# Optimization experiments

Measured on AMD Instinct MI355X. Metric: run time of the kernel, lower is better.

Reference implementation:

```python
import jax, jax.numpy as jnp
import numpy as np

GRID_SIZE = 16
NUM_VOXELS = GRID_SIZE ** 3


def setup_inputs() -> dict:
    key = jax.random.key(0)
    k1, k2, k3 = jax.random.split(key, 3)
    B, D, N = 4, 128, 100000
    features = jax.random.normal(k1, (B, D, N), dtype=jnp.float32)
    xyz_normalized = jax.random.uniform(k2, (B, N, 3), dtype=jnp.float32)
    mask = jax.random.randint(k3, (B, N), 0, 2, dtype=jnp.int32)
    return {"features": features, "xyz_normalized": xyz_normalized, "mask": mask}


def _flat_voxel_idx(xyz):
    # xyz: [B, N, 3] in [0,1); voxel index per point, flattened z*G*G + y*G + x
    G = GRID_SIZE
    vi = jnp.clip((xyz * G).astype(jnp.int32), 0, G - 1)  # [B, N, 3]
    return vi[..., 2] * (G * G) + vi[..., 1] * G + vi[..., 0]  # [B, N]


def reference(features, xyz_normalized, mask):
    # features: [B, D, N], xyz_normalized: [B, N, 3], mask: [B, N] int (0/1)
    idx = _flat_voxel_idx(xyz_normalized)  # [B, N]
    feats = features * mask[:, None, :].astype(features.dtype)  # [B, D, N]

    def per_batch(f_dn, idx_n, m_n):
        # scatter-add features: segment_sum over points -> [V, D] -> [D, V]
        sums = jax.ops.segment_sum(f_dn.T, idx_n, num_segments=NUM_VOXELS)  # [V, D]
        counts = jax.ops.segment_sum(m_n, idx_n, num_segments=NUM_VOXELS)  # [V]
        counts = jnp.maximum(counts, 1).astype(f_dn.dtype)
        return (sums / counts[:, None]).T  # [D, V]

    return jax.vmap(per_batch)(feats, idx, mask)  # [B, D, V]
```

## Files before the change

kernel.cpp:

```cpp
#include <hip/hip_runtime.h>

#define GSZ   16
#define NVOX  4096
#define BB    4
#define DD    128
#define PThr  256
#define PPT   16
#define PTILE (PThr * PPT)

typedef __fp16 half2v __attribute__((ext_vector_type(2)));

__device__ __forceinline__ void lds_pk_add_f16(unsigned byte_off, float va, float vb) {
    half2v h = __builtin_amdgcn_cvt_pkrtz(va, vb);
    unsigned hv;
    __builtin_memcpy(&hv, &h, 4);
    asm volatile("ds_pk_add_f16 %0, %1" : : "v"(byte_off), "v"(hv) : "memory");
}

__global__ __launch_bounds__(PThr) void k_prep(const float* __restrict__ xyz,
                                               const int* __restrict__ mask,
                                               unsigned short* __restrict__ idxm,
                                               unsigned short* __restrict__ histg,
                                               int N, int NT) {
    __shared__ unsigned int hist[NVOX];
    const int tile = blockIdx.x, b = blockIdx.y;
    for (int j = threadIdx.x; j < NVOX; j += PThr) hist[j] = 0u;
    __syncthreads();

    const float*    xb = xyz  + (size_t)b * N * 3;
    const int*      mb = mask + (size_t)b * N;
    unsigned short* ib = idxm + (size_t)b * N;

    const int p0 = tile * PTILE + (int)threadIdx.x * PPT;

    if (p0 + PPT <= N) {
        float a[3 * PPT];
        float4* av = (float4*)a;
        const float4* xv = (const float4*)(xb + 3 * (size_t)p0);
#pragma unroll
        for (int q = 0; q < 12; q++) av[q] = xv[q];
        int mk[PPT];
        const int4* mv = (const int4*)(mb + p0);
#pragma unroll
        for (int q = 0; q < 4; q++) {
            int4 m4 = mv[q];
            mk[4*q+0] = m4.x; mk[4*q+1] = m4.y; mk[4*q+2] = m4.z; mk[4*q+3] = m4.w;
        }
        alignas(16) unsigned short pk[PPT];
#pragma unroll
        for (int k = 0; k < PPT; k++) {
            int vx = min(max((int)(a[3*k+0] * (float)GSZ), 0), GSZ - 1);
            int vy = min(max((int)(a[3*k+1] * (float)GSZ), 0), GSZ - 1);
            int vz = min(max((int)(a[3*k+2] * (float)GSZ), 0), GSZ - 1);
            int idx = vz * GSZ * GSZ + vy * GSZ + vx;
            if (mk[k] != 0) {
                pk[k] = (unsigned short)idx;
                atomicAdd(&hist[idx], 1u);
            } else {
                pk[k] = 0xFFFFu;
            }
        }
        uint4* dst = (uint4*)(ib + p0);
        dst[0] = ((const uint4*)pk)[0];
        dst[1] = ((const uint4*)pk)[1];
    } else {
        for (int k = 0; k < PPT; k++) {
            int p = p0 + k;
            if (p >= N) break;
            float x = xb[3*(size_t)p+0], y = xb[3*(size_t)p+1], z = xb[3*(size_t)p+2];
            int vx = min(max((int)(x * (float)GSZ), 0), GSZ - 1);
            int vy = min(max((int)(y * (float)GSZ), 0), GSZ - 1);
            int vz = min(max((int)(z * (float)GSZ), 0), GSZ - 1);
            int idx = vz * GSZ * GSZ + vy * GSZ + vx;
            if (mb[p] != 0) { ib[p] = (unsigned short)idx; atomicAdd(&hist[idx], 1u); }
            else            { ib[p] = 0xFFFFu; }
        }
    }
    __syncthreads();
    unsigned short* hg = histg + ((size_t)b * NT + tile) * NVOX;
    for (int j = threadIdx.x; j < NVOX; j += PThr) hg[j] = (unsigned short)hist[j];
}

__global__ __launch_bounds__(1024) void k_scatter(const float* __restrict__ feats,
                                                  const unsigned short* __restrict__ idxm,
                                                  const unsigned short* __restrict__ histg,
                                                  float* __restrict__ out, int N, int NT) {
    __shared__ half2v acc[NVOX];
    const int dp = blockIdx.x & 63;
    const int b  = blockIdx.x >> 6;
    const int d0 = dp * 2;

    {
        half2v z = { (__fp16)0.f, (__fp16)0.f };
        for (int j = threadIdx.x; j < NVOX; j += 1024) acc[j] = z;
    }
    __syncthreads();

    const unsigned short* ib = idxm + (size_t)b * N;
    const float* f0 = feats + ((size_t)b * DD + (size_t)d0) * (size_t)N;
    const float* f1 = f0 + N;
    const unsigned accbase = (unsigned)(size_t)(void*)&acc[0];

#define PROC(idx_, va_, vb_)                                       \
    {                                                              \
        unsigned _i = (idx_);                                      \
        if (_i != 0xFFFFu) lds_pk_add_f16(accbase + _i * 4u, (va_), (vb_)); \
    }

    const int stride = 1024 * 8;
    const int niter  = N / stride;
    const int t8     = (int)threadIdx.x * 8;

    if (niter > 0) {
        uint4  iv = *(const uint4*)(ib + t8);
        float4 a0 = *(const float4*)(f0 + t8);
        float4 a1 = *(const float4*)(f0 + t8 + 4);
        float4 b0 = *(const float4*)(f1 + t8);
        float4 b1 = *(const float4*)(f1 + t8 + 4);
        for (int it = 0; it < niter; it++) {
            int inext = (it + 1 < niter) ? (it + 1) * stride + t8 : t8;
            uint4  ivn = *(const uint4*)(ib + inext);
            float4 a0n = *(const float4*)(f0 + inext);
            float4 a1n = *(const float4*)(f0 + inext + 4);
            float4 b0n = *(const float4*)(f1 + inext);
            float4 b1n = *(const float4*)(f1 + inext + 4);

            PROC(iv.x & 0xFFFFu, a0.x, b0.x)
            PROC(iv.x >> 16,     a0.y, b0.y)
            PROC(iv.y & 0xFFFFu, a0.z, b0.z)
            PROC(iv.y >> 16,     a0.w, b0.w)
            PROC(iv.z & 0xFFFFu, a1.x, b1.x)
            PROC(iv.z >> 16,     a1.y, b1.y)
            PROC(iv.w & 0xFFFFu, a1.z, b1.z)
            PROC(iv.w >> 16,     a1.w, b1.w)

            iv = ivn; a0 = a0n; a1 = a1n; b0 = b0n; b1 = b1n;
        }
    }
    for (int p = niter * stride + (int)threadIdx.x; p < N; p += 1024) {
        unsigned id = ib[p];
        if (id != 0xFFFFu) lds_pk_add_f16(accbase + id * 4u, f0[p], f1[p]);
    }
#undef PROC

    const int v0 = (int)threadIdx.x * 4;
    int c0 = 0, c1 = 0, c2 = 0, c3 = 0;
    {
        const unsigned short* hb = histg + (size_t)b * NT * NVOX + v0;
        for (int t = 0; t < NT; t++) {
            ushort4 h = *(const ushort4*)(hb + (size_t)t * NVOX);
            c0 += h.x; c1 += h.y; c2 += h.z; c3 += h.w;
        }
    }
    __syncthreads();

    half2v s0 = acc[v0+0], s1 = acc[v0+1], s2 = acc[v0+2], s3 = acc[v0+3];
    float i0 = 1.f / (float)max(c0, 1);
    float i1 = 1.f / (float)max(c1, 1);
    float i2 = 1.f / (float)max(c2, 1);
    float i3 = 1.f / (float)max(c3, 1);
    float4 oa, ob;
    oa.x = (float)s0.x * i0;  ob.x = (float)s0.y * i0;
    oa.y = (float)s1.x * i1;  ob.y = (float)s1.y * i1;
    oa.z = (float)s2.x * i2;  ob.z = (float)s2.y * i2;
    oa.w = (float)s3.x * i3;  ob.w = (float)s3.y * i3;
    float* r0 = out + ((size_t)b * DD + (size_t)d0) * (size_t)NVOX + v0;
    *(float4*)r0          = oa;
    *(float4*)(r0 + NVOX) = ob;
}

extern "C" void kernel_launch(void* const* d_in, const int* in_sizes, int n_in,
                              void* d_out, int out_size, void* d_ws, size_t ws_size,
                              hipStream_t stream) {
    const float* feats = (const float*)d_in[0];
    const float* xyz   = (const float*)d_in[1];
    const int*   mask  = (const int*)d_in[2];
    float*       out   = (float*)d_out;

    int N  = in_sizes[2] / BB;
    int NT = (N + PTILE - 1) / PTILE;

    char* w = (char*)d_ws;
    unsigned short* idxm  = (unsigned short*)w;
    w += (((size_t)BB * N * sizeof(unsigned short)) + 255) & ~(size_t)255;
    unsigned short* histg = (unsigned short*)w;

    k_prep   <<<dim3(NT, BB), PThr, 0, stream>>>(xyz, mask, idxm, histg, N, NT);
    k_scatter<<<BB * (DD / 2), 1024, 0, stream>>>(feats, idxm, histg, out, N, NT);
}
```

Measured before the change: 302.8 us.

## Split scatter over point slices with partial LDS histograms and a combine pass

The scatter kernel now splits each (batch, feature pair) job into 4 point slices, so it launches 1024 blocks of 512 threads instead of 256 blocks of 1024 threads. This gives more parallelism across the GPU's compute units. Each block writes its fp16 partial sums to a workspace. A new combine kernel adds the partials, and a separate counts kernel precomputes the reciprocal counts. The prep kernel also uses 1024 threads with 4 points each, and the explicit prefetch in the scatter loop is dropped. The cost is extra partial-buffer traffic and two more kernel launches.

New measurement: 307.5 us. No clear change (+1.6%).

```diff
diff --git a/kernel.cpp b/kernel.cpp
--- a/kernel.cpp
+++ b/kernel.cpp
@@ -4,9 +4,11 @@
 #define NVOX  4096
 #define BB    4
 #define DD    128
-#define PThr  256
-#define PPT   16
+#define PThr  1024
+#define PPT   4
 #define PTILE (PThr * PPT)
+#define SS    4
+#define SThr  512
 
 typedef __fp16 half2v __attribute__((ext_vector_type(2)));
 
@@ -38,15 +40,10 @@
         float4* av = (float4*)a;
         const float4* xv = (const float4*)(xb + 3 * (size_t)p0);
 #pragma unroll
-        for (int q = 0; q < 12; q++) av[q] = xv[q];
-        int mk[PPT];
-        const int4* mv = (const int4*)(mb + p0);
-#pragma unroll
-        for (int q = 0; q < 4; q++) {
-            int4 m4 = mv[q];
-            mk[4*q+0] = m4.x; mk[4*q+1] = m4.y; mk[4*q+2] = m4.z; mk[4*q+3] = m4.w;
-        }
-        alignas(16) unsigned short pk[PPT];
+        for (int q = 0; q < 3; q++) av[q] = xv[q];
+        int4 m4 = *(const int4*)(mb + p0);
+        int mk[PPT] = { m4.x, m4.y, m4.z, m4.w };
+        alignas(8) unsigned short pk[PPT];
 #pragma unroll
         for (int k = 0; k < PPT; k++) {
             int vx = min(max((int)(a[3*k+0] * (float)GSZ), 0), GSZ - 1);
@@ -60,9 +57,7 @@
                 pk[k] = 0xFFFFu;
             }
         }
-        uint4* dst = (uint4*)(ib + p0);
-        dst[0] = ((const uint4*)pk)[0];
-        dst[1] = ((const uint4*)pk)[1];
+        *(uint2*)(ib + p0) = *(const uint2*)pk;
     } else {
         for (int k = 0; k < PPT; k++) {
             int p = p0 + k;
@@ -81,20 +76,43 @@
     for (int j = threadIdx.x; j < NVOX; j += PThr) hg[j] = (unsigned short)hist[j];
 }
 
-__global__ __launch_bounds__(1024) void k_scatter(const float* __restrict__ feats,
-                                                  const unsigned short* __restrict__ idxm,
-                                                  const unsigned short* __restrict__ histg,
-                                                  float* __restrict__ out, int N, int NT) {
+__global__ __launch_bounds__(1024) void k_counts(const unsigned short* __restrict__ histg,
+                                                 float* __restrict__ rinv, int NT) {
+    const int gid = blockIdx.x * 1024 + (int)threadIdx.x;
+    const int b = gid >> 12, v = gid & (NVOX - 1);
+    const unsigned short* hb = histg + (size_t)b * NT * NVOX + v;
+    int c = 0, t = 0;
+    for (; t + 4 <= NT; t += 4) {
+        int c0 = hb[(size_t)(t+0)*NVOX];
+        int c1 = hb[(size_t)(t+1)*NVOX];
+        int c2 = hb[(size_t)(t+2)*NVOX];
+        int c3 = hb[(size_t)(t+3)*NVOX];
+        c += c0 + c1 + c2 + c3;
+    }
+    for (; t < NT; t++) c += hb[(size_t)t*NVOX];
+    rinv[gid] = 1.0f / (float)max(c, 1);
+}
+
+__global__ __launch_bounds__(SThr, 6) void k_scatter(const float* __restrict__ feats,
+                                                     const unsigned short* __restrict__ idxm,
+                                                     unsigned int* __restrict__ partial,
+                                                     int N, int Q) {
     __shared__ half2v acc[NVOX];
-    const int dp = blockIdx.x & 63;
-    const int b  = blockIdx.x >> 6;
-    const int d0 = dp * 2;
+    const int bid = blockIdx.x;
+    const int dp  = bid & 63;
+    const int b   = (bid >> 6) & (BB - 1);
+    const int s   = bid >> 8;
+    const int d0  = dp * 2;
 
     {
         half2v z = { (__fp16)0.f, (__fp16)0.f };
-        for (int j = threadIdx.x; j < NVOX; j += 1024) acc[j] = z;
-    }
-    __syncthreads();
+        for (int j = threadIdx.x; j < NVOX; j += SThr) acc[j] = z;
+    }
+    __syncthreads();
+
+    const int start = s * Q;
+    const int end   = min(start + Q, N);
+    const int cnt   = end - start;
 
     const unsigned short* ib = idxm + (size_t)b * N;
     const float* f0 = feats + ((size_t)b * DD + (size_t)d0) * (size_t)N;
@@ -107,63 +125,73 @@
         if (_i != 0xFFFFu) lds_pk_add_f16(accbase + _i * 4u, (va_), (vb_)); \
     }
 
-    const int stride = 1024 * 8;
-    const int niter  = N / stride;
-    const int t8     = (int)threadIdx.x * 8;
-
-    if (niter > 0) {
-        uint4  iv = *(const uint4*)(ib + t8);
-        float4 a0 = *(const float4*)(f0 + t8);
-        float4 a1 = *(const float4*)(f0 + t8 + 4);
-        float4 b0 = *(const float4*)(f1 + t8);
-        float4 b1 = *(const float4*)(f1 + t8 + 4);
-        for (int it = 0; it < niter; it++) {
-            int inext = (it + 1 < niter) ? (it + 1) * stride + t8 : t8;
-            uint4  ivn = *(const uint4*)(ib + inext);
-            float4 a0n = *(const float4*)(f0 + inext);
-            float4 a1n = *(const float4*)(f0 + inext + 4);
-            float4 b0n = *(const float4*)(f1 + inext);
-            float4 b1n = *(const float4*)(f1 + inext + 4);
-
-            PROC(iv.x & 0xFFFFu, a0.x, b0.x)
-            PROC(iv.x >> 16,     a0.y, b0.y)
-            PROC(iv.y & 0xFFFFu, a0.z, b0.z)
-            PROC(iv.y >> 16,     a0.w, b0.w)
-            PROC(iv.z & 0xFFFFu, a1.x, b1.x)
-            PROC(iv.z >> 16,     a1.y, b1.y)
-            PROC(iv.w & 0xFFFFu, a1.z, b1.z)
-            PROC(iv.w >> 16,     a1.w, b1.w)
-
-            iv = ivn; a0 = a0n; a1 = a1n; b0 = b0n; b1 = b1n;
-        }
-    }
-    for (int p = niter * stride + (int)threadIdx.x; p < N; p += 1024) {
+    const int nfull = cnt > 0 ? cnt / (SThr * 8) : 0;
+    const int t8    = (int)threadIdx.x * 8;
+
+    for (int it = 0; it < nfull; it++) {
+        const int p = start + it * (SThr * 8) + t8;
+        uint4  iv = *(const uint4*)(ib + p);
+        float4 a0 = *(const float4*)(f0 + p);
+        float4 a1 = *(const float4*)(f0 + p + 4);
+        float4 b0 = *(const float4*)(f1 + p);
+        float4 b1 = *(const float4*)(f1 + p + 4);
+
+        PROC(iv.x & 0xFFFFu, a0.x, b0.x)
+        PROC(iv.x >> 16,     a0.y, b0.y)
+        PROC(iv.y & 0xFFFFu, a0.z, b0.z)
+        PROC(iv.y >> 16,     a0.w, b0.w)
+        PROC(iv.z & 0xFFFFu, a1.x, b1.x)
+        PROC(iv.z >> 16,     a1.y, b1.y)
+        PROC(iv.w & 0xFFFFu, a1.z, b1.z)
+        PROC(iv.w >> 16,     a1.w, b1.w)
+    }
+    for (int p = start + nfull * (SThr * 8) + (int)threadIdx.x; p < end; p += SThr) {
         unsigned id = ib[p];
         if (id != 0xFFFFu) lds_pk_add_f16(accbase + id * 4u, f0[p], f1[p]);
     }
 #undef PROC
 
-    const int v0 = (int)threadIdx.x * 4;
-    int c0 = 0, c1 = 0, c2 = 0, c3 = 0;
-    {
-        const unsigned short* hb = histg + (size_t)b * NT * NVOX + v0;
-        for (int t = 0; t < NT; t++) {
-            ushort4 h = *(const ushort4*)(hb + (size_t)t * NVOX);
-            c0 += h.x; c1 += h.y; c2 += h.z; c3 += h.w;
+    __syncthreads();
+
+    unsigned int* pb = partial + (size_t)bid * NVOX;
+    for (int j = threadIdx.x; j < NVOX; j += SThr) {
+        half2v h = acc[j];
+        unsigned w;
+        __builtin_memcpy(&w, &h, 4);
+        pb[j] = w;
+    }
+}
+
+__global__ __launch_bounds__(1024) void k_combine(const unsigned int* __restrict__ partial,
+                                                  const float* __restrict__ rinv,
+                                                  float* __restrict__ out) {
+    const int bid = blockIdx.x;
+    const int dp  = bid & 63;
+    const int b   = bid >> 6;
+    const int d0  = dp * 2;
+    const int v0  = (int)threadIdx.x * 4;
+
+    float s0[4] = {0.f, 0.f, 0.f, 0.f};
+    float s1[4] = {0.f, 0.f, 0.f, 0.f};
+#pragma unroll
+    for (int s = 0; s < SS; s++) {
+        uint4 P = *(const uint4*)(partial + ((size_t)(s * BB * 64 + bid)) * NVOX + v0);
+        unsigned w[4] = { P.x, P.y, P.z, P.w };
+#pragma unroll
+        for (int j = 0; j < 4; j++) {
+            half2v h;
+            __builtin_memcpy(&h, &w[j], 4);
+            s0[j] += (float)h.x;
+            s1[j] += (float)h.y;
         }
     }
-    __syncthreads();
-
-    half2v s0 = acc[v0+0], s1 = acc[v0+1], s2 = acc[v0+2], s3 = acc[v0+3];
-    float i0 = 1.f / (float)max(c0, 1);
-    float i1 = 1.f / (float)max(c1, 1);
-    float i2 = 1.f / (float)max(c2, 1);
-    float i3 = 1.f / (float)max(c3, 1);
+    float4 rv = *(const float4*)(rinv + (size_t)b * NVOX + v0);
+    float r[4] = { rv.x, rv.y, rv.z, rv.w };
     float4 oa, ob;
-    oa.x = (float)s0.x * i0;  ob.x = (float)s0.y * i0;
-    oa.y = (float)s1.x * i1;  ob.y = (float)s1.y * i1;
-    oa.z = (float)s2.x * i2;  ob.z = (float)s2.y * i2;
-    oa.w = (float)s3.x * i3;  ob.w = (float)s3.y * i3;
+    oa.x = s0[0]*r[0];  ob.x = s1[0]*r[0];
+    oa.y = s0[1]*r[1];  ob.y = s1[1]*r[1];
+    oa.z = s0[2]*r[2];  ob.z = s1[2]*r[2];
+    oa.w = s0[3]*r[3];  ob.w = s1[3]*r[3];
     float* r0 = out + ((size_t)b * DD + (size_t)d0) * (size_t)NVOX + v0;
     *(float4*)r0          = oa;
     *(float4*)(r0 + NVOX) = ob;
@@ -179,12 +207,19 @@
 
     int N  = in_sizes[2] / BB;
     int NT = (N + PTILE - 1) / PTILE;
+    int Q  = (((N + SS - 1) / SS) + 7) & ~7;
 
     char* w = (char*)d_ws;
     unsigned short* idxm  = (unsigned short*)w;
     w += (((size_t)BB * N * sizeof(unsigned short)) + 255) & ~(size_t)255;
     unsigned short* histg = (unsigned short*)w;
+    w += (((size_t)BB * NT * NVOX * sizeof(unsigned short)) + 255) & ~(size_t)255;
+    float*          rinv  = (float*)w;
+    w += (((size_t)BB * NVOX * sizeof(float)) + 255) & ~(size_t)255;
+    unsigned int*   part  = (unsigned int*)w;
 
     k_prep   <<<dim3(NT, BB), PThr, 0, stream>>>(xyz, mask, idxm, histg, N, NT);
-    k_scatter<<<BB * (DD / 2), 1024, 0, stream>>>(feats, idxm, histg, out, N, NT);
-}
+    k_scatter<<<SS * BB * (DD / 2), SThr, 0, stream>>>(feats, idxm, part, N, Q);
+    k_counts <<<(BB * NVOX) / 1024, 1024, 0, stream>>>(histg, rinv, NT);
+    k_combine<<<BB * (DD / 2), 1024, 0, stream>>>(part, rinv, out);
+}
```
